# Kernel tuning notes

Measured on AMD Instinct MI355X. Metric: run time of the kernel, lower is better.

## Reference

```python
import jax, jax.numpy as jnp
import numpy as np

N_FEATURES = 40
H = 64
N_CLASSES = 3
N_NODES = 100000
N_EDGES = 3200000
THRESHOLD = 0.5


def setup_inputs() -> dict:
    key = jax.random.key(0)
    ks = jax.random.split(key, 8)
    x = jax.random.normal(ks[0], (N_NODES, N_FEATURES), dtype=jnp.float32)
    edge_index = jax.random.randint(ks[1], (2, N_EDGES), 0, N_NODES, dtype=jnp.int64)
    s1 = 1.0 / np.sqrt(N_FEATURES)
    s2 = 1.0 / np.sqrt(H)
    W1 = jax.random.uniform(ks[2], (N_FEATURES, H), jnp.float32, -s1, s1)
    b1 = jnp.zeros((H,), jnp.float32)
    Wf = jax.random.uniform(ks[3], (H, H), jnp.float32, -s2, s2)
    bf = jax.random.uniform(ks[4], (H,), jnp.float32, -s2, s2)
    W2 = jax.random.uniform(ks[5], (H, N_CLASSES), jnp.float32, -s2, s2)
    b2 = jnp.zeros((N_CLASSES,), jnp.float32)
    ethical_filter = jnp.ones((N_CLASSES,), jnp.float32)
    return {"x": x, "edge_index": edge_index, "W1": W1, "b1": b1,
            "Wf": Wf, "bf": bf, "W2": W2, "b2": b2,
            "ethical_filter": ethical_filter}


def _gcn_conv(x, W, b, src, dst, n_nodes):
    # PyG GCNConv: add self-loops, symmetric normalization, src->dst aggregate.
    h = x @ W                                   # [N, F_out]
    loop = jnp.arange(n_nodes, dtype=src.dtype)
    s = jnp.concatenate([src, loop])            # [E+N]
    d = jnp.concatenate([dst, loop])
    deg = jnp.zeros((n_nodes,), h.dtype).at[d].add(1.0)
    dinv = jax.lax.rsqrt(deg)                   # deg >= 1 due to self-loops
    norm = dinv[s] * dinv[d]                    # [E+N]
    msg = h[s] * norm[:, None]                  # gather + scale
    out = jnp.zeros((n_nodes, h.shape[1]), h.dtype).at[d].add(msg)
    return out + b


def reference(x, edge_index, W1, b1, Wf, bf, W2, b2, ethical_filter):
    n = x.shape[0]
    src, dst = edge_index[0], edge_index[1]
    h = jax.nn.relu(_gcn_conv(x, W1, b1, src, dst, n))
    # SpikingNeuron: mem = fc(h); spike = (mem >= threshold).float()
    spike = (h @ Wf + bf >= THRESHOLD).astype(x.dtype)
    out = _gcn_conv(spike, W2, b2, src, dst, n)
    return out * ethical_filter
```

## Files before the change

### kernel.cpp

```cpp
#include <hip/hip_runtime.h>

#define NF 40
#define NF4 10
#define H  64
#define NC 3
#define BK 256
#define CAP 10240
#define MAXNBK 512
#define SMASK 0xFFFFFu
#define EPB 6400

__device__ __forceinline__ void add4(float4& a, const float4& u) {
    a.x += u.x; a.y += u.y; a.z += u.z; a.w += u.w;
}

__global__ void k_zero(int* __restrict__ p, int n) {
    int i = blockIdx.x * blockDim.x + threadIdx.x;
    if (i < n) p[i] = 0;
}

__global__ __launch_bounds__(512) void k_bin2(const int* __restrict__ src,
                                              const int* __restrict__ dst,
                                              int* __restrict__ gcur,
                                              unsigned* __restrict__ staging,
                                              int ne, int nbk) {
    __shared__ unsigned sorted[EPB];
    __shared__ unsigned short sbk[EPB];
    __shared__ int cnt[MAXNBK];
    __shared__ int tsum[MAXNBK];
    __shared__ int lstart[MAXNBK];
    __shared__ int gbase[MAXNBK];
    __shared__ int cur[MAXNBK];
    int t = threadIdx.x;
    int e0 = blockIdx.x * EPB;
    int m = min(EPB, ne - e0);
    if (m <= 0) return;

    for (int b = t; b < MAXNBK; b += 512) cnt[b] = 0;
    __syncthreads();
    for (int j = t; j < m; j += 512)
        atomicAdd(&cnt[dst[e0 + j] >> 8], 1);
    __syncthreads();
    int val = (t < nbk) ? cnt[t] : 0;
    tsum[t] = val;
    __syncthreads();
    for (int off = 1; off < 512; off <<= 1) {
        int a = (t >= off) ? tsum[t - off] : 0;
        __syncthreads();
        tsum[t] += a;
        __syncthreads();
    }
    lstart[t] = tsum[t] - val;
    cur[t] = tsum[t] - val;
    if (t < nbk) gbase[t] = val ? atomicAdd(&gcur[t], val) : 0;
    __syncthreads();
    for (int j = t; j < m; j += 512) {
        int d = dst[e0 + j], s = src[e0 + j];
        int b = d >> 8;
        int p = atomicAdd(&cur[b], 1);
        sorted[p] = ((unsigned)(d & 255) << 20) | (unsigned)s;
        sbk[p] = (unsigned short)b;
    }
    __syncthreads();
    for (int j = t; j < m; j += 512) {
        int b = sbk[j];
        staging[(size_t)b * CAP + gbase[b] + (j - lstart[b])] = sorted[j];
    }
}

__global__ __launch_bounds__(512) void k_sort(unsigned* __restrict__ staging,
                                              const int* __restrict__ gcur,
                                              int* __restrict__ rs, int* __restrict__ rl,
                                              float* __restrict__ dinv, int n) {
    __shared__ unsigned buf[CAP];
    __shared__ int cnt[BK];
    __shared__ int scn[BK];
    __shared__ int cur[BK];
    int b = blockIdx.x, t = threadIdx.x;
    int ebase = b * CAP;
    int rlen = gcur[b];
    for (int j = t; j < rlen; j += 512) buf[j] = staging[ebase + j];
    if (t < BK) cnt[t] = 0;
    __syncthreads();
    for (int j = t; j < rlen; j += 512)
        atomicAdd(&cnt[buf[j] >> 20], 1);
    __syncthreads();
    if (t < BK) scn[t] = cnt[t];
    __syncthreads();
    for (int off = 1; off < BK; off <<= 1) {
        int a = (t < BK && t >= off) ? scn[t - off] : 0;
        __syncthreads();
        if (t < BK) scn[t] += a;
        __syncthreads();
    }
    if (t < BK) {
        int deg = cnt[t];
        int excl = scn[t] - deg;
        cur[t] = excl;
        int node = b * BK + t;
        if (node < n) {
            rs[node] = ebase + excl;
            rl[node] = deg;
            dinv[node] = rsqrtf((float)(deg + 1));
        }
    }
    __syncthreads();
    for (int j = t; j < rlen; j += 512) {
        unsigned e = buf[j];
        int p = atomicAdd(&cur[e >> 20], 1);
        staging[ebase + p] = e;
    }
}

__global__ __launch_bounds__(256) void k_pull1(
        const unsigned* __restrict__ st, const int* __restrict__ rs,
        const int* __restrict__ rl, const float* __restrict__ dinv,
        const float4* __restrict__ x4, float4* __restrict__ ax4, int n) {
    __shared__ float4 red[4][64];
    int t = threadIdx.x;
    int w = t >> 6, lane = t & 63;
    int d = blockIdx.x * 4 + w;
    if (d >= n) return;
    int g = lane / 10, f = lane - g * 10;
    int beg = rs[d], len = rl[d];
    float dd = dinv[d];
    float4 acc = make_float4(0.f, 0.f, 0.f, 0.f);
    if (g < 6) {
        int j = beg + g, end = beg + len;
        for (; j + 6 < end; j += 12) {
            unsigned eA = st[j], eB = st[j + 6];
            int sA = (int)(eA & SMASK), sB = (int)(eB & SMASK);
            float wA = dinv[sA], wB = dinv[sB];
            float4 a4 = x4[sA * NF4 + f];
            float4 b4 = x4[sB * NF4 + f];
            acc.x += a4.x * wA + b4.x * wB;
            acc.y += a4.y * wA + b4.y * wB;
            acc.z += a4.z * wA + b4.z * wB;
            acc.w += a4.w * wA + b4.w * wB;
        }
        if (j < end) {
            unsigned e = st[j];
            int s = (int)(e & SMASK);
            float wv = dinv[s];
            float4 v = x4[s * NF4 + f];
            acc.x += v.x * wv; acc.y += v.y * wv;
            acc.z += v.z * wv; acc.w += v.w * wv;
        }
    }
    red[w][lane] = acc;
    if (lane < NF4) {
        float4 tot = red[w][lane];
        #pragma unroll
        for (int gg = 1; gg < 6; ++gg) add4(tot, red[w][gg * 10 + lane]);
        float4 self = x4[d * NF4 + lane];
        float4 o;
        o.x = dd * (tot.x + self.x * dd);
        o.y = dd * (tot.y + self.y * dd);
        o.z = dd * (tot.z + self.z * dd);
        o.w = dd * (tot.w + self.w * dd);
        ax4[d * NF4 + lane] = o;
    }
}

__global__ __launch_bounds__(256) void k_node(
        const float4* __restrict__ ax4,
        const float* __restrict__ W1, const float* __restrict__ b1,
        const float* __restrict__ Wf, const float* __restrict__ bf,
        const float* __restrict__ W2, const float* __restrict__ dinv,
        float4* __restrict__ s2sp4, int n) {
    __shared__ float hT[4][H * 32];
    int t = threadIdx.x, w = t >> 6, lane = t & 63;
    int r = lane & 7, c = lane >> 3;

    int nb0 = (blockIdx.x * 4 + w) * 32;
    if (nb0 >= n) return;
    int cnt = min(32, n - nb0);

    float bb[8], bfv[8], w2s[8][3];
    #pragma unroll
    for (int j = 0; j < 8; ++j) {
        bb[j]  = b1[8 * c + j];
        bfv[j] = bf[8 * c + j];
        w2s[j][0] = W2[(8 * c + j) * NC + 0];
        w2s[j][1] = W2[(8 * c + j) * NC + 1];
        w2s[j][2] = W2[(8 * c + j) * NC + 2];
    }

    float* axT = &hT[w][0];
    #pragma unroll
    for (int i = 0; i < 5; ++i) {
        int idx = lane + 64 * i;
        int no = idx / NF4, q = idx - no * NF4;
        float4 a = make_float4(0.f, 0.f, 0.f, 0.f);
        if (no < cnt) a = ax4[(size_t)(nb0 + no) * NF4 + q];
        axT[(4 * q + 0) * 32 + no] = a.x;
        axT[(4 * q + 1) * 32 + no] = a.y;
        axT[(4 * q + 2) * 32 + no] = a.z;
        axT[(4 * q + 3) * 32 + no] = a.w;
    }

    float acc[4][8];
    #pragma unroll
    for (int i = 0; i < 4; ++i)
        #pragma unroll
        for (int j = 0; j < 8; ++j) acc[i][j] = bb[j];
    for (int k = 0; k < NF; ++k) {
        float4 a   = *(const float4*)&axT[k * 32 + 4 * r];
        float4 blo = *(const float4*)&W1[k * H + 8 * c];
        float4 bhi = *(const float4*)&W1[k * H + 8 * c + 4];
        float av[4] = {a.x, a.y, a.z, a.w};
        float bv[8] = {blo.x, blo.y, blo.z, blo.w, bhi.x, bhi.y, bhi.z, bhi.w};
        #pragma unroll
        for (int i = 0; i < 4; ++i)
            #pragma unroll
            for (int j = 0; j < 8; ++j) acc[i][j] = fmaf(av[i], bv[j], acc[i][j]);
    }
    #pragma unroll
    for (int j = 0; j < 8; ++j) {
        float4 hv = make_float4(fmaxf(acc[0][j], 0.f), fmaxf(acc[1][j], 0.f),
                                fmaxf(acc[2][j], 0.f), fmaxf(acc[3][j], 0.f));
        *(float4*)&hT[w][(8 * c + j) * 32 + 4 * r] = hv;
    }

    float acc2[4][8];
    #pragma unroll
    for (int i = 0; i < 4; ++i)
        #pragma unroll
        for (int j = 0; j < 8; ++j) acc2[i][j] = bfv[j];
    for (int k = 0; k < H; ++k) {
        float4 a   = *(const float4*)&hT[w][k * 32 + 4 * r];
        float4 blo = *(const float4*)&Wf[k * H + 8 * c];
        float4 bhi = *(const float4*)&Wf[k * H + 8 * c + 4];
        float av[4] = {a.x, a.y, a.z, a.w};
        float bv[8] = {blo.x, blo.y, blo.z, blo.w, bhi.x, bhi.y, bhi.z, bhi.w};
        #pragma unroll
        for (int i = 0; i < 4; ++i)
            #pragma unroll
            for (int j = 0; j < 8; ++j) acc2[i][j] = fmaf(av[i], bv[j], acc2[i][j]);
    }

    float p0[4], p1[4], p2[4];
    #pragma unroll
    for (int i = 0; i < 4; ++i) { p0[i] = 0.f; p1[i] = 0.f; p2[i] = 0.f; }
    #pragma unroll
    for (int i = 0; i < 4; ++i)
        #pragma unroll
        for (int j = 0; j < 8; ++j) {
            float s = (acc2[i][j] >= 0.5f) ? 1.f : 0.f;
            p0[i] = fmaf(s, w2s[j][0], p0[i]);
            p1[i] = fmaf(s, w2s[j][1], p1[i]);
            p2[i] = fmaf(s, w2s[j][2], p2[i]);
        }
    #pragma unroll
    for (int off = 8; off < 64; off <<= 1) {
        #pragma unroll
        for (int i = 0; i < 4; ++i) {
            p0[i] += __shfl_xor(p0[i], off);
            p1[i] += __shfl_xor(p1[i], off);
            p2[i] += __shfl_xor(p2[i], off);
        }
    }
    if (c == 0) {
        #pragma unroll
        for (int i = 0; i < 4; ++i) {
            int no = 4 * r + i;
            if (no < cnt) {
                int node = nb0 + no;
                float di = dinv[node];
                s2sp4[node] = make_float4(p0[i] * di, p1[i] * di, p2[i] * di, 0.f);
            }
        }
    }
}

__global__ __launch_bounds__(256) void k_pull2(
        const unsigned* __restrict__ st, const int* __restrict__ rs,
        const int* __restrict__ rl, const float* __restrict__ dinv,
        const float4* __restrict__ s2sp4, const float* __restrict__ b2,
        const float* __restrict__ ef, float* __restrict__ out, int n) {
    int t = threadIdx.x;
    int w = t >> 6, lane = t & 63;
    int d = blockIdx.x * 4 + w;
    if (d >= n) return;
    int beg = rs[d], end = beg + rl[d];
    float a0 = 0.f, a1 = 0.f, a2 = 0.f;
    for (int j = beg + lane; j < end; j += 64) {
        float4 v = s2sp4[st[j] & SMASK];
        a0 += v.x; a1 += v.y; a2 += v.z;
    }
    for (int off = 32; off; off >>= 1) {
        a0 += __shfl_down(a0, off);
        a1 += __shfl_down(a1, off);
        a2 += __shfl_down(a2, off);
    }
    if (lane == 0) {
        float dd = dinv[d];
        float4 self = s2sp4[d];
        out[d * NC + 0] = (dd * (a0 + self.x) + b2[0]) * ef[0];
        out[d * NC + 1] = (dd * (a1 + self.y) + b2[1]) * ef[1];
        out[d * NC + 2] = (dd * (a2 + self.z) + b2[2]) * ef[2];
    }
}

extern "C" void kernel_launch(void* const* d_in, const int* in_sizes, int n_in,
                              void* d_out, int out_size, void* d_ws, size_t ws_size,
                              hipStream_t stream) {
    const float* x  = (const float*)d_in[0];
    const int*   ei = (const int*)d_in[1];
    const float* W1 = (const float*)d_in[2];
    const float* b1 = (const float*)d_in[3];
    const float* Wf = (const float*)d_in[4];
    const float* bf = (const float*)d_in[5];
    const float* W2 = (const float*)d_in[6];
    const float* b2 = (const float*)d_in[7];
    const float* ef = (const float*)d_in[8];

    int n  = in_sizes[0] / NF;
    int ne = in_sizes[1] / 2;
    const int* src = ei;
    const int* dst = ei + ne;
    int nbk = (n + BK - 1) >> 8;

    auto al = [](size_t v) { return (v + 255) & ~(size_t)255; };
    char* ws = (char*)d_ws;
    size_t off = 0;
    unsigned* staging = (unsigned*)(ws + off); off += al((size_t)nbk * CAP * 4);
    float*    axbuf   = (float*)(ws + off);    off += al((size_t)n * NF * 4);
    float*    s2sp    = (float*)(ws + off);    off += al((size_t)n * 4 * 4);
    float*    dinv    = (float*)(ws + off);    off += al((size_t)n * 4);
    int*      rsb     = (int*)(ws + off);      off += al((size_t)n * 4);
    int*      rlb     = (int*)(ws + off);      off += al((size_t)n * 4);
    int*      gcur    = (int*)(ws + off);      off += al((size_t)MAXNBK * 4);
    float* out = (float*)d_out;

    int binblocks = (ne + EPB - 1) / EPB;

    k_zero <<<2, 256, 0, stream>>>(gcur, MAXNBK);
    k_bin2 <<<binblocks, 512, 0, stream>>>(src, dst, gcur, staging, ne, nbk);
    k_sort <<<nbk, 512, 0, stream>>>(staging, gcur, rsb, rlb, dinv, n);
    k_pull1<<<(n + 3) / 4, 256, 0, stream>>>(staging, rsb, rlb, dinv,
                                             (const float4*)x, (float4*)axbuf, n);
    k_node <<<(n + 127) / 128, 256, 0, stream>>>(
        (const float4*)axbuf, W1, b1, Wf, bf, W2, dinv, (float4*)s2sp, n);
    k_pull2<<<(n + 3) / 4, 256, 0, stream>>>(staging, rsb, rlb, dinv, (const float4*)s2sp,
                                             b2, ef, out, n);
}
```

Before: 221.4 us.

## Fuse first-layer gather into node MLP kernel and halve pull2 wave width

```diff
diff --git a/kernel.cpp b/kernel.cpp
--- a/kernel.cpp
+++ b/kernel.cpp
@@ -9,10 +9,6 @@
 #define MAXNBK 512
 #define SMASK 0xFFFFFu
 #define EPB 6400
-
-__device__ __forceinline__ void add4(float4& a, const float4& u) {
-    a.x += u.x; a.y += u.y; a.z += u.z; a.w += u.w;
-}
 
 __global__ void k_zero(int* __restrict__ p, int n) {
     int i = blockIdx.x * blockDim.x + threadIdx.x;
@@ -112,70 +108,83 @@
     }
 }
 
-__global__ __launch_bounds__(256) void k_pull1(
+__global__ __launch_bounds__(256, 4) void k_fused(
         const unsigned* __restrict__ st, const int* __restrict__ rs,
         const int* __restrict__ rl, const float* __restrict__ dinv,
-        const float4* __restrict__ x4, float4* __restrict__ ax4, int n) {
-    __shared__ float4 red[4][64];
-    int t = threadIdx.x;
-    int w = t >> 6, lane = t & 63;
-    int d = blockIdx.x * 4 + w;
-    if (d >= n) return;
-    int g = lane / 10, f = lane - g * 10;
-    int beg = rs[d], len = rl[d];
-    float dd = dinv[d];
-    float4 acc = make_float4(0.f, 0.f, 0.f, 0.f);
-    if (g < 6) {
-        int j = beg + g, end = beg + len;
-        for (; j + 6 < end; j += 12) {
-            unsigned eA = st[j], eB = st[j + 6];
-            int sA = (int)(eA & SMASK), sB = (int)(eB & SMASK);
-            float wA = dinv[sA], wB = dinv[sB];
-            float4 a4 = x4[sA * NF4 + f];
-            float4 b4 = x4[sB * NF4 + f];
-            acc.x += a4.x * wA + b4.x * wB;
-            acc.y += a4.y * wA + b4.y * wB;
-            acc.z += a4.z * wA + b4.z * wB;
-            acc.w += a4.w * wA + b4.w * wB;
-        }
-        if (j < end) {
-            unsigned e = st[j];
-            int s = (int)(e & SMASK);
-            float wv = dinv[s];
-            float4 v = x4[s * NF4 + f];
-            acc.x += v.x * wv; acc.y += v.y * wv;
-            acc.z += v.z * wv; acc.w += v.w * wv;
-        }
-    }
-    red[w][lane] = acc;
-    if (lane < NF4) {
-        float4 tot = red[w][lane];
-        #pragma unroll
-        for (int gg = 1; gg < 6; ++gg) add4(tot, red[w][gg * 10 + lane]);
-        float4 self = x4[d * NF4 + lane];
-        float4 o;
-        o.x = dd * (tot.x + self.x * dd);
-        o.y = dd * (tot.y + self.y * dd);
-        o.z = dd * (tot.z + self.z * dd);
-        o.w = dd * (tot.w + self.w * dd);
-        ax4[d * NF4 + lane] = o;
-    }
-}
-
-__global__ __launch_bounds__(256) void k_node(
-        const float4* __restrict__ ax4,
+        const float4* __restrict__ x4,
         const float* __restrict__ W1, const float* __restrict__ b1,
         const float* __restrict__ Wf, const float* __restrict__ bf,
-        const float* __restrict__ W2, const float* __restrict__ dinv,
-        float4* __restrict__ s2sp4, int n) {
+        const float* __restrict__ W2, float4* __restrict__ s2sp4, int n) {
     __shared__ float hT[4][H * 32];
     int t = threadIdx.x, w = t >> 6, lane = t & 63;
-    int r = lane & 7, c = lane >> 3;
-
+    int g = lane / 10, f = lane - g * 10;
     int nb0 = (blockIdx.x * 4 + w) * 32;
     if (nb0 >= n) return;
     int cnt = min(32, n - nb0);
-
+    float* axT = &hT[w][0];
+    float4 z = make_float4(0.f, 0.f, 0.f, 0.f);
+
+    for (int no = 0; no < cnt; ++no) {
+        int d = nb0 + no;
+        int beg = rs[d], len = rl[d];
+        float dd = dinv[d];
+        float4 acc = z;
+        if (g < 6) {
+            int j = beg + g, end = beg + len;
+            if (j < end) {
+                unsigned e0 = st[j];
+                bool p1 = (j + 6 < end);
+                unsigned e1 = p1 ? st[j + 6] : 0u;
+                int s0 = (int)(e0 & SMASK), s1 = (int)(e1 & SMASK);
+                float w0 = dinv[s0];
+                float w1 = p1 ? dinv[s1] : 0.f;
+                float4 v0 = x4[(size_t)s0 * NF4 + f];
+                float4 v1 = p1 ? x4[(size_t)s1 * NF4 + f] : z;
+                j += 12;
+                while (j < end) {
+                    unsigned f0 = st[j];
+                    bool q1 = (j + 6 < end);
+                    unsigned f1 = q1 ? st[j + 6] : 0u;
+                    acc.x += v0.x * w0 + v1.x * w1;
+                    acc.y += v0.y * w0 + v1.y * w1;
+                    acc.z += v0.z * w0 + v1.z * w1;
+                    acc.w += v0.w * w0 + v1.w * w1;
+                    int t0 = (int)(f0 & SMASK), t1 = (int)(f1 & SMASK);
+                    w0 = dinv[t0];
+                    w1 = q1 ? dinv[t1] : 0.f;
+                    v0 = x4[(size_t)t0 * NF4 + f];
+                    v1 = q1 ? x4[(size_t)t1 * NF4 + f] : z;
+                    j += 12;
+                }
+                acc.x += v0.x * w0 + v1.x * w1;
+                acc.y += v0.y * w0 + v1.y * w1;
+                acc.z += v0.z * w0 + v1.z * w1;
+                acc.w += v0.w * w0 + v1.w * w1;
+            }
+        }
+        float4 t1v;
+        t1v.x = acc.x + __shfl(acc.x, lane + 30);
+        t1v.y = acc.y + __shfl(acc.y, lane + 30);
+        t1v.z = acc.z + __shfl(acc.z, lane + 30);
+        t1v.w = acc.w + __shfl(acc.w, lane + 30);
+        float4 tot;
+        tot.x = t1v.x + __shfl(t1v.x, lane + 10) + __shfl(t1v.x, lane + 20);
+        tot.y = t1v.y + __shfl(t1v.y, lane + 10) + __shfl(t1v.y, lane + 20);
+        tot.z = t1v.z + __shfl(t1v.z, lane + 10) + __shfl(t1v.z, lane + 20);
+        tot.w = t1v.w + __shfl(t1v.w, lane + 10) + __shfl(t1v.w, lane + 20);
+        if (lane < NF4) {
+            float4 self = x4[(size_t)d * NF4 + lane];
+            axT[(4 * lane + 0) * 32 + no] = dd * (tot.x + self.x * dd);
+            axT[(4 * lane + 1) * 32 + no] = dd * (tot.y + self.y * dd);
+            axT[(4 * lane + 2) * 32 + no] = dd * (tot.z + self.z * dd);
+            axT[(4 * lane + 3) * 32 + no] = dd * (tot.w + self.w * dd);
+        }
+    }
+    if (cnt < 32 && lane < NF)
+        for (int no2 = cnt; no2 < 32; ++no2)
+            axT[lane * 32 + no2] = 0.f;
+
+    int r = lane & 7, c = lane >> 3;
     float bb[8], bfv[8], w2s[8][3];
     #pragma unroll
     for (int j = 0; j < 8; ++j) {
@@ -186,24 +195,11 @@
         w2s[j][2] = W2[(8 * c + j) * NC + 2];
     }
 
-    float* axT = &hT[w][0];
-    #pragma unroll
-    for (int i = 0; i < 5; ++i) {
-        int idx = lane + 64 * i;
-        int no = idx / NF4, q = idx - no * NF4;
-        float4 a = make_float4(0.f, 0.f, 0.f, 0.f);
-        if (no < cnt) a = ax4[(size_t)(nb0 + no) * NF4 + q];
-        axT[(4 * q + 0) * 32 + no] = a.x;
-        axT[(4 * q + 1) * 32 + no] = a.y;
-        axT[(4 * q + 2) * 32 + no] = a.z;
-        axT[(4 * q + 3) * 32 + no] = a.w;
-    }
-
-    float acc[4][8];
+    float acc1[4][8];
     #pragma unroll
     for (int i = 0; i < 4; ++i)
         #pragma unroll
-        for (int j = 0; j < 8; ++j) acc[i][j] = bb[j];
+        for (int j = 0; j < 8; ++j) acc1[i][j] = bb[j];
     for (int k = 0; k < NF; ++k) {
         float4 a   = *(const float4*)&axT[k * 32 + 4 * r];
         float4 blo = *(const float4*)&W1[k * H + 8 * c];
@@ -213,12 +209,12 @@
         #pragma unroll
         for (int i = 0; i < 4; ++i)
             #pragma unroll
-            for (int j = 0; j < 8; ++j) acc[i][j] = fmaf(av[i], bv[j], acc[i][j]);
+            for (int j = 0; j < 8; ++j) acc1[i][j] = fmaf(av[i], bv[j], acc1[i][j]);
     }
     #pragma unroll
     for (int j = 0; j < 8; ++j) {
-        float4 hv = make_float4(fmaxf(acc[0][j], 0.f), fmaxf(acc[1][j], 0.f),
-                                fmaxf(acc[2][j], 0.f), fmaxf(acc[3][j], 0.f));
+        float4 hv = make_float4(fmaxf(acc1[0][j], 0.f), fmaxf(acc1[1][j], 0.f),
+                                fmaxf(acc1[2][j], 0.f), fmaxf(acc1[3][j], 0.f));
         *(float4*)&hT[w][(8 * c + j) * 32 + 4 * r] = hv;
     }
 
@@ -280,20 +276,22 @@
         const float* __restrict__ ef, float* __restrict__ out, int n) {
     int t = threadIdx.x;
     int w = t >> 6, lane = t & 63;
-    int d = blockIdx.x * 4 + w;
+    int half = lane >> 5, sl = lane & 31;
+    int d = blockIdx.x * 8 + w * 2 + half;
     if (d >= n) return;
     int beg = rs[d], end = beg + rl[d];
     float a0 = 0.f, a1 = 0.f, a2 = 0.f;
-    for (int j = beg + lane; j < end; j += 64) {
+    for (int j = beg + sl; j < end; j += 32) {
         float4 v = s2sp4[st[j] & SMASK];
         a0 += v.x; a1 += v.y; a2 += v.z;
     }
-    for (int off = 32; off; off >>= 1) {
-        a0 += __shfl_down(a0, off);
-        a1 += __shfl_down(a1, off);
-        a2 += __shfl_down(a2, off);
-    }
-    if (lane == 0) {
+    #pragma unroll
+    for (int off = 16; off; off >>= 1) {
+        a0 += __shfl_down(a0, off, 32);
+        a1 += __shfl_down(a1, off, 32);
+        a2 += __shfl_down(a2, off, 32);
+    }
+    if (sl == 0) {
         float dd = dinv[d];
         float4 self = s2sp4[d];
         out[d * NC + 0] = (dd * (a0 + self.x) + b2[0]) * ef[0];
@@ -325,7 +323,6 @@
     char* ws = (char*)d_ws;
     size_t off = 0;
     unsigned* staging = (unsigned*)(ws + off); off += al((size_t)nbk * CAP * 4);
-    float*    axbuf   = (float*)(ws + off);    off += al((size_t)n * NF * 4);
     float*    s2sp    = (float*)(ws + off);    off += al((size_t)n * 4 * 4);
     float*    dinv    = (float*)(ws + off);    off += al((size_t)n * 4);
     int*      rsb     = (int*)(ws + off);      off += al((size_t)n * 4);
@@ -338,10 +335,9 @@
     k_zero <<<2, 256, 0, stream>>>(gcur, MAXNBK);
     k_bin2 <<<binblocks, 512, 0, stream>>>(src, dst, gcur, staging, ne, nbk);
     k_sort <<<nbk, 512, 0, stream>>>(staging, gcur, rsb, rlb, dinv, n);
-    k_pull1<<<(n + 3) / 4, 256, 0, stream>>>(staging, rsb, rlb, dinv,
-                                             (const float4*)x, (float4*)axbuf, n);
-    k_node <<<(n + 127) / 128, 256, 0, stream>>>(
-        (const float4*)axbuf, W1, b1, Wf, bf, W2, dinv, (float4*)s2sp, n);
-    k_pull2<<<(n + 3) / 4, 256, 0, stream>>>(staging, rsb, rlb, dinv, (const float4*)s2sp,
-                                             b2, ef, out, n);
-}
+    k_fused<<<(n + 127) / 128, 256, 0, stream>>>(staging, rsb, rlb, dinv,
+                                                 (const float4*)x, W1, b1, Wf, bf, W2,
+                                                 (float4*)s2sp, n);
+    k_pull2<<<(n + 7) / 8, 256, 0, stream>>>(staging, rsb, rlb, dinv,
+                                             (const float4*)s2sp, b2, ef, out, n);
+}
```

Measured after the change: 233.2 us. 1.05x slower.
